# Kernel tuning notes

Hardware: AMD Instinct MI355X
Metric: run time of the kernel (lower is better)

Reference implementation:

```python
import jax, jax.numpy as jnp
import numpy as np

B, C, H, W = 16, 3, 384, 1280
EPS = 1e-7


def setup_inputs() -> dict:
    key = jax.random.key(0)
    k1, k2, k3, k4 = jax.random.split(key, 4)
    source_image = jax.random.normal(k1, (B, C, H, W), jnp.float32)
    depth_map = jax.random.uniform(k2, (B, 1, H, W), jnp.float32, minval=0.1, maxval=80.0)
    pose = 0.05 * jax.random.normal(k3, (B, 6), jnp.float32)
    # realistic KITTI-style pinhole intrinsics, per-batch mild perturbation
    base = jnp.array([[0.58 * W, 0.0, 0.5 * W],
                      [0.0, 1.92 * H, 0.5 * H],
                      [0.0, 0.0, 1.0]], jnp.float32)
    noise = 1.0 + 0.01 * jax.random.normal(k4, (B, 3, 3), jnp.float32)
    intrinsic = base[None] * noise  # zero entries stay zero -> invertible
    return {"source_image": source_image, "depth_map": depth_map,
            "pose": pose, "intrinsic": intrinsic}


def rot_from_axisangle(aa):
    # aa: [B,3] -> [B,3,3] (Rodrigues)
    theta = jnp.linalg.norm(aa, axis=-1, keepdims=True)  # [B,1]
    axis = aa / (theta + EPS)
    c = jnp.cos(theta)
    s = jnp.sin(theta)
    t = 1.0 - c
    x, y, z = axis[:, 0:1], axis[:, 1:2], axis[:, 2:3]
    row0 = jnp.concatenate([t * x * x + c, t * x * y - s * z, t * z * x + s * y], axis=1)
    row1 = jnp.concatenate([t * x * y + s * z, t * y * y + c, t * y * z - s * x], axis=1)
    row2 = jnp.concatenate([t * z * x - s * y, t * y * z + s * x, t * z * z + c], axis=1)
    return jnp.stack([row0, row1, row2], axis=1)  # [B,3,3]


def bilinear_grid_sample(img, gx, gy):
    # img: [B,C,H,W]; gx,gy: [B,H,W] in [-1,1]; align_corners=True, padding zeros
    Bc, Cc, Hc, Wc = img.shape
    x = (gx + 1.0) * 0.5 * (Wc - 1)
    y = (gy + 1.0) * 0.5 * (Hc - 1)
    x0 = jnp.floor(x)
    y0 = jnp.floor(y)
    x1 = x0 + 1.0
    y1 = y0 + 1.0
    wx1 = x - x0
    wx0 = 1.0 - wx1
    wy1 = y - y0
    wy0 = 1.0 - wy1
    imgf = img.reshape(Bc, Cc, Hc * Wc)

    def gather(xi, yi):
        inb = ((xi >= 0) & (xi <= Wc - 1) & (yi >= 0) & (yi <= Hc - 1)).astype(img.dtype)
        xc = jnp.clip(xi, 0, Wc - 1).astype(jnp.int32)
        yc = jnp.clip(yi, 0, Hc - 1).astype(jnp.int32)
        idx = (yc * Wc + xc).reshape(Bc, 1, -1)
        vals = jnp.take_along_axis(imgf, jnp.broadcast_to(idx, (Bc, Cc, idx.shape[-1])), axis=2)
        return vals.reshape(Bc, Cc, Hc, Wc) * inb[:, None]

    out = (gather(x0, y0) * (wx0 * wy0)[:, None]
           + gather(x1, y0) * (wx1 * wy0)[:, None]
           + gather(x0, y1) * (wx0 * wy1)[:, None]
           + gather(x1, y1) * (wx1 * wy1)[:, None])
    return out


def reference(source_image, depth_map, pose, intrinsic):
    Bb, _, Hh, Ww = depth_map.shape
    # pixel grid, homogeneous [H,W,3] = (x, y, 1)
    ys, xs = jnp.meshgrid(jnp.arange(Hh, dtype=depth_map.dtype),
                          jnp.arange(Ww, dtype=depth_map.dtype), indexing='ij')
    pix = jnp.stack([xs, ys, jnp.ones_like(xs)], axis=-1)  # [H,W,3]
    # backproject: K^{-1} @ pix * depth
    inv_K = jnp.linalg.inv(intrinsic)  # [B,3,3]
    cam = jnp.einsum('bij,hwj->bhwi', inv_K, pix)  # [B,H,W,3]
    frustum = cam * jnp.transpose(depth_map, (0, 2, 3, 1))  # [B,H,W,3]
    # rigid transform
    R = rot_from_axisangle(pose[:, :3])  # [B,3,3]
    t = pose[:, 3:]  # [B,3]
    points = jnp.einsum('bij,bhwj->bhwi', R, frustum) + t[:, None, None, :]
    # project with K
    coord = jnp.einsum('bij,bhwj->bhwi', intrinsic, points)  # [B,H,W,3]
    z = coord[..., 2] + EPS
    px = coord[..., 0] / z
    py = coord[..., 1] / z
    gx = px / (Ww - 1) * 2.0 - 1.0
    gy = py / (Hh - 1) * 2.0 - 1.0
    return bilinear_grid_sample(source_image, gx, gy)
```

## Files before the change

### kernel.cpp

```cpp
#include <hip/hip_runtime.h>

#define B_ 16
#define C_ 3
#define H_ 384
#define W_ 1280
#define HW_ (H_*W_)
#define EPS_ 1e-7f

#define COLS_ 256
#define ROWS_ 2
#define BANDS_ (W_/COLS_)
#define RTILES_ (H_/ROWS_)
#define NBLK_ (BANDS_*RTILES_*B_)
#define NXCD_ 8

typedef float v2f __attribute__((ext_vector_type(2)));

__device__ __forceinline__ v2f load2(const float* p) {
  v2f r;
  __builtin_memcpy(&r, p, 8);
  return r;
}

__device__ __forceinline__ void mat3mul(const float* A, const float* Bm, float* C) {
  #pragma unroll
  for (int i = 0; i < 3; i++)
    #pragma unroll
    for (int j = 0; j < 3; j++)
      C[i*3+j] = A[i*3+0]*Bm[0*3+j] + A[i*3+1]*Bm[1*3+j] + A[i*3+2]*Bm[2*3+j];
}

__device__ void compute_MT(const float* __restrict__ pose,
                           const float* __restrict__ intr,
                           int b, float* M, float* T)
{
  float K[9];
  #pragma unroll
  for (int i = 0; i < 9; i++) K[i] = intr[b*9 + i];
  float aa0 = pose[b*6 + 0], aa1 = pose[b*6 + 1], aa2 = pose[b*6 + 2];
  float t0  = pose[b*6 + 3], t1  = pose[b*6 + 4], t2  = pose[b*6 + 5];

  float theta = sqrtf(aa0*aa0 + aa1*aa1 + aa2*aa2);
  float invn  = 1.0f / (theta + EPS_);
  float x = aa0*invn, y = aa1*invn, z = aa2*invn;
  float c = cosf(theta), s = sinf(theta), t = 1.0f - c;
  float R[9] = {
    t*x*x + c,   t*x*y - s*z, t*z*x + s*y,
    t*x*y + s*z, t*y*y + c,   t*y*z - s*x,
    t*z*x - s*y, t*y*z + s*x, t*z*z + c
  };

  float a = K[0], bb = K[1], cc = K[2];
  float d = K[3], e  = K[4], f  = K[5];
  float g = K[6], h  = K[7], ii = K[8];
  float A0 = e*ii - f*h, A1 = f*g - d*ii, A2 = d*h - e*g;
  float id = 1.0f / (a*A0 + bb*A1 + cc*A2);
  float iK[9] = {
    A0*id, (cc*h - bb*ii)*id, (bb*f - cc*e)*id,
    A1*id, (a*ii - cc*g)*id,  (cc*d - a*f)*id,
    A2*id, (bb*g - a*h)*id,   (a*e  - bb*d)*id
  };

  float KR[9];
  mat3mul(K, R, KR);
  mat3mul(KR, iK, M);
  T[0] = K[0]*t0 + K[1]*t1 + K[2]*t2;
  T[1] = K[3]*t0 + K[4]*t1 + K[5]*t2;
  T[2] = K[6]*t0 + K[7]*t1 + K[8]*t2;
}

__global__ __launch_bounds__(256) void warp_kernel(
    const float* __restrict__ src,
    const float* __restrict__ depth,
    const float* __restrict__ pose,
    const float* __restrict__ intr,
    float* __restrict__ out)
{
  __shared__ float sp[12];

  int l = blockIdx.x;
  int w = (l & (NXCD_-1)) * (NBLK_/NXCD_) + (l >> 3);
  int rt   = w % RTILES_;
  int tmp  = w / RTILES_;
  int band = tmp % BANDS_;
  int b    = tmp / BANDS_;

  if (threadIdx.x == 0) {
    float M[9], T[3];
    compute_MT(pose, intr, b, M, T);
    #pragma unroll
    for (int i = 0; i < 9; i++) sp[i] = M[i];
    #pragma unroll
    for (int i = 0; i < 3; i++) sp[9 + i] = T[i];
  }
  __syncthreads();
  float m00 = sp[0], m01 = sp[1], m02 = sp[2];
  float m10 = sp[3], m11 = sp[4], m12 = sp[5];
  float m20 = sp[6], m21 = sp[7], m22 = sp[8];
  float T0  = sp[9], T1  = sp[10], T2 = sp[11];

  int j  = band * COLS_ + threadIdx.x;
  int i0 = rt * ROWS_;
  float xf = (float)j;

  float ax = m00*xf + m02;
  float ay = m10*xf + m12;
  float az = m20*xf + m22;

  size_t sb = (size_t)b * C_ * HW_;
  const float* s0p = src + sb;
  const float* s1p = s0p + HW_;
  const float* s2p = s1p + HW_;

  const float* dp = depth + (size_t)b * HW_ + (size_t)i0 * W_ + j;
  float dv[ROWS_];
  #pragma unroll
  for (int r = 0; r < ROWS_; r++)
    dv[r] = __builtin_nontemporal_load(dp + r * W_);

  #pragma unroll
  for (int r = 0; r < ROWS_; r++) {
    int i = i0 + r;
    float yf = (float)i;
    float d  = dv[r];

    float cx = (ax + m01*yf)*d + T0;
    float cy = (ay + m11*yf)*d + T1;
    float cz = (az + m21*yf)*d + T2;
    float inv = 1.0f / (cz + EPS_);
    float px = cx * inv;
    float py = cy * inv;

    float x0f = floorf(px), y0f = floorf(py);
    float x1f = x0f + 1.0f, y1f = y0f + 1.0f;
    float wx1 = px - x0f, wx0 = 1.0f - wx1;
    float wy1 = py - y0f, wy0 = 1.0f - wy1;

    float mx0 = (x0f >= 0.0f && x0f <= (float)(W_-1)) ? 1.0f : 0.0f;
    float mx1 = (x1f >= 0.0f && x1f <= (float)(W_-1)) ? 1.0f : 0.0f;
    float my0 = (y0f >= 0.0f && y0f <= (float)(H_-1)) ? 1.0f : 0.0f;
    float my1 = (y1f >= 0.0f && y1f <= (float)(H_-1)) ? 1.0f : 0.0f;

    int xc0 = (int)fminf(fmaxf(x0f, 0.0f), (float)(W_-1));
    int xc1 = (int)fminf(fmaxf(x1f, 0.0f), (float)(W_-1));
    int yc0 = (int)fminf(fmaxf(y0f, 0.0f), (float)(H_-1));
    int yc1 = (int)fminf(fmaxf(y1f, 0.0f), (float)(H_-1));

    float w00 = wx0*wy0*mx0*my0;
    float w01 = wx1*wy0*mx1*my0;
    float w10 = wx0*wy1*mx0*my1;
    float w11 = wx1*wy1*mx1*my1;

    int base = xc0 < (W_-2) ? xc0 : (W_-2);
    bool sl0 = (xc0 == base);
    bool sl1 = (xc1 == base + 1);
    float wax = (sl0 ? w00 : 0.0f) + (sl1 ? 0.0f : w01);
    float way = (sl0 ? 0.0f : w00) + (sl1 ? w01 : 0.0f);
    float wbx = (sl0 ? w10 : 0.0f) + (sl1 ? 0.0f : w11);
    float wby = (sl0 ? 0.0f : w10) + (sl1 ? w11 : 0.0f);

    int rb0 = yc0*W_ + base;
    int rb1 = yc1*W_ + base;

    v2f a0 = load2(s0p + rb0);
    v2f b0 = load2(s0p + rb1);
    v2f a1 = load2(s1p + rb0);
    v2f b1 = load2(s1p + rb1);
    v2f a2 = load2(s2p + rb0);
    v2f b2 = load2(s2p + rb1);

    float v0 = a0.x*wax + a0.y*way + b0.x*wbx + b0.y*wby;
    float v1 = a1.x*wax + a1.y*way + b1.x*wbx + b1.y*wby;
    float v2 = a2.x*wax + a2.y*way + b2.x*wbx + b2.y*wby;

    size_t op = (size_t)i * W_ + j;
    __builtin_nontemporal_store(v0, &out[sb + op]);
    __builtin_nontemporal_store(v1, &out[sb + HW_ + op]);
    __builtin_nontemporal_store(v2, &out[sb + 2*(size_t)HW_ + op]);
  }
}

extern "C" void kernel_launch(void* const* d_in, const int* in_sizes, int n_in,
                              void* d_out, int out_size, void* d_ws, size_t ws_size,
                              hipStream_t stream) {
  const float* src   = (const float*)d_in[0];
  const float* depth = (const float*)d_in[1];
  const float* pose  = (const float*)d_in[2];
  const float* intr  = (const float*)d_in[3];
  float* out = (float*)d_out;

  dim3 grid(NBLK_);
  warp_kernel<<<grid, 256, 0, stream>>>(src, depth, pose, intr, out);
}
```

Measured before the change: 251.8 us.

## Process two adjacent pixels per thread sharing a 4-wide source gather window

Each thread now handles two horizontally adjacent output pixels in one row instead of one pixel in each of two rows. A single pair of 4-float source loads per channel serves both bilinear samples, with an extra row load when the second pixel's rows differ and a scalar fallback when its footprint falls outside the window. Depth loads and output stores become 2-wide vectors. The aim is fewer gather instructions and better memory coalescing, at the cost of more select logic, divergent fallback branches and wider 16-byte loads that may be unaligned.

Result: slower. 280.7 us (+11.5%).

```diff
diff --git a/kernel.cpp b/kernel.cpp
--- a/kernel.cpp
+++ b/kernel.cpp
@@ -15,11 +15,20 @@
 #define NXCD_ 8
 
 typedef float v2f __attribute__((ext_vector_type(2)));
+typedef float v4f __attribute__((ext_vector_type(4)));
 
 __device__ __forceinline__ v2f load2(const float* p) {
-  v2f r;
-  __builtin_memcpy(&r, p, 8);
-  return r;
+  v2f r; __builtin_memcpy(&r, p, 8); return r;
+}
+__device__ __forceinline__ v4f load4(const float* p) {
+  v4f r; __builtin_memcpy(&r, p, 16); return r;
+}
+__device__ __forceinline__ void storent2(float* p, float a, float b) {
+  v2f r; r.x = a; r.y = b;
+  __builtin_nontemporal_store(r, (v2f*)p);
+}
+__device__ __forceinline__ float dot4(v4f a, v4f b) {
+  return a.x*b.x + a.y*b.y + a.z*b.z + a.w*b.w;
 }
 
 __device__ __forceinline__ void mat3mul(const float* A, const float* Bm, float* C) {
@@ -69,6 +78,32 @@
   T[2] = K[6]*t0 + K[7]*t1 + K[8]*t2;
 }
 
+__device__ __forceinline__ void project_px(
+    float xf, float yf, float d,
+    float m00,float m01,float m02,float m10,float m11,float m12,
+    float m20,float m21,float m22,float T0,float T1,float T2,
+    float& wx0,float& wx1,float& wy0,float& wy1,
+    int& xc0,int& xc1,int& yc0,int& yc1)
+{
+  float cz = (m20*xf + m21*yf + m22)*d + T2;
+  float inv = 1.0f / (cz + EPS_);
+  float px = ((m00*xf + m01*yf + m02)*d + T0) * inv;
+  float py = ((m10*xf + m11*yf + m12)*d + T1) * inv;
+  float x0f = floorf(px), y0f = floorf(py);
+  float fx1 = px - x0f, fx0 = 1.0f - fx1;
+  float fy1 = py - y0f, fy0 = 1.0f - fy1;
+  float mx0 = (x0f >= 0.0f && x0f <= (float)(W_-1)) ? 1.0f : 0.0f;
+  float mx1 = (x0f+1.0f >= 0.0f && x0f+1.0f <= (float)(W_-1)) ? 1.0f : 0.0f;
+  float my0 = (y0f >= 0.0f && y0f <= (float)(H_-1)) ? 1.0f : 0.0f;
+  float my1 = (y0f+1.0f >= 0.0f && y0f+1.0f <= (float)(H_-1)) ? 1.0f : 0.0f;
+  wx0 = fx0*mx0; wx1 = fx1*mx1;
+  wy0 = fy0*my0; wy1 = fy1*my1;
+  xc0 = (int)fminf(fmaxf(x0f, 0.0f), (float)(W_-1));
+  xc1 = (int)fminf(fmaxf(x0f+1.0f, 0.0f), (float)(W_-1));
+  yc0 = (int)fminf(fmaxf(y0f, 0.0f), (float)(H_-1));
+  yc1 = (int)fminf(fmaxf(y0f+1.0f, 0.0f), (float)(H_-1));
+}
+
 __global__ __launch_bounds__(256) void warp_kernel(
     const float* __restrict__ src,
     const float* __restrict__ depth,
@@ -85,13 +120,22 @@
   int band = tmp % BANDS_;
   int b    = tmp / BANDS_;
 
-  if (threadIdx.x == 0) {
+  int t  = threadIdx.x;
+  int cp = t & 127;
+  int rr = t >> 7;
+  int j0 = band * COLS_ + 2*cp;
+  int i  = rt * ROWS_ + rr;
+
+  const float* dpp = depth + (size_t)b * HW_ + (size_t)i * W_ + j0;
+  v2f dpair = load2(dpp);
+
+  if (t == 0) {
     float M[9], T[3];
     compute_MT(pose, intr, b, M, T);
     #pragma unroll
-    for (int i = 0; i < 9; i++) sp[i] = M[i];
+    for (int k = 0; k < 9; k++) sp[k] = M[k];
     #pragma unroll
-    for (int i = 0; i < 3; i++) sp[9 + i] = T[i];
+    for (int k = 0; k < 3; k++) sp[9 + k] = T[k];
   }
   __syncthreads();
   float m00 = sp[0], m01 = sp[1], m02 = sp[2];
@@ -99,85 +143,86 @@
   float m20 = sp[6], m21 = sp[7], m22 = sp[8];
   float T0  = sp[9], T1  = sp[10], T2 = sp[11];
 
-  int j  = band * COLS_ + threadIdx.x;
-  int i0 = rt * ROWS_;
-  float xf = (float)j;
-
-  float ax = m00*xf + m02;
-  float ay = m10*xf + m12;
-  float az = m20*xf + m22;
+  float yf = (float)i;
+
+  float wxA0,wxA1,wyA0,wyA1, wxB0,wxB1,wyB0,wyB1;
+  int xcA0,xcA1,ycA0,ycA1, xcB0,xcB1,ycB0,ycB1;
+  project_px((float)j0,     yf, dpair.x, m00,m01,m02,m10,m11,m12,m20,m21,m22,T0,T1,T2,
+             wxA0,wxA1,wyA0,wyA1, xcA0,xcA1,ycA0,ycA1);
+  project_px((float)(j0+1), yf, dpair.y, m00,m01,m02,m10,m11,m12,m20,m21,m22,T0,T1,T2,
+             wxB0,wxB1,wyB0,wyB1, xcB0,xcB1,ycB0,ycB1);
+
+  int baseA = xcA0 < (W_-2) ? xcA0 : (W_-2);
+  int bp    = baseA < (W_-4) ? baseA : (W_-4);
+  int pA0 = xcA0 - bp, pA1 = xcA1 - bp;
+  int pB0 = xcB0 - bp, pB1 = xcB1 - bp;
+
+  int R0 = ycA0, R1 = ycA1;
+  int sB0 = (ycB0 == R0) ? 0 : ((ycB0 == R1) ? 1 : 2);
+  int sB1 = (ycB1 == R1) ? 1 : ((ycB1 == R0) ? 0 : 2);
+  bool needE = (sB0 == 2) || (sB1 == 2);
+  bool fb = (pB1 > 3) || (pB0 < 0) || ((sB0 == 2) && (sB1 == 2));
+  int yE = (sB0 == 2) ? ycB0 : ycB1;
+
+  float u0 = (sB0 == 0 ? wyB0 : 0.0f) + (sB1 == 0 ? wyB1 : 0.0f);
+  float u1 = (sB0 == 1 ? wyB0 : 0.0f) + (sB1 == 1 ? wyB1 : 0.0f);
+  float u2 = (sB0 == 2 ? wyB0 : 0.0f) + (sB1 == 2 ? wyB1 : 0.0f);
+
+  v4f wA0v, wA1v, wB0v, wB1v, wB2v;
+  #pragma unroll
+  for (int k = 0; k < 4; k++) {
+    float wva = (pA0 == k ? wxA0 : 0.0f) + (pA1 == k ? wxA1 : 0.0f);
+    float wvb = (pB0 == k ? wxB0 : 0.0f) + (pB1 == k ? wxB1 : 0.0f);
+    wA0v[k] = wva * wyA0;
+    wA1v[k] = wva * wyA1;
+    wB0v[k] = wvb * u0;
+    wB1v[k] = wvb * u1;
+    wB2v[k] = wvb * u2;
+  }
 
   size_t sb = (size_t)b * C_ * HW_;
   const float* s0p = src + sb;
   const float* s1p = s0p + HW_;
   const float* s2p = s1p + HW_;
-
-  const float* dp = depth + (size_t)b * HW_ + (size_t)i0 * W_ + j;
-  float dv[ROWS_];
-  #pragma unroll
-  for (int r = 0; r < ROWS_; r++)
-    dv[r] = __builtin_nontemporal_load(dp + r * W_);
-
-  #pragma unroll
-  for (int r = 0; r < ROWS_; r++) {
-    int i = i0 + r;
-    float yf = (float)i;
-    float d  = dv[r];
-
-    float cx = (ax + m01*yf)*d + T0;
-    float cy = (ay + m11*yf)*d + T1;
-    float cz = (az + m21*yf)*d + T2;
-    float inv = 1.0f / (cz + EPS_);
-    float px = cx * inv;
-    float py = cy * inv;
-
-    float x0f = floorf(px), y0f = floorf(py);
-    float x1f = x0f + 1.0f, y1f = y0f + 1.0f;
-    float wx1 = px - x0f, wx0 = 1.0f - wx1;
-    float wy1 = py - y0f, wy0 = 1.0f - wy1;
-
-    float mx0 = (x0f >= 0.0f && x0f <= (float)(W_-1)) ? 1.0f : 0.0f;
-    float mx1 = (x1f >= 0.0f && x1f <= (float)(W_-1)) ? 1.0f : 0.0f;
-    float my0 = (y0f >= 0.0f && y0f <= (float)(H_-1)) ? 1.0f : 0.0f;
-    float my1 = (y1f >= 0.0f && y1f <= (float)(H_-1)) ? 1.0f : 0.0f;
-
-    int xc0 = (int)fminf(fmaxf(x0f, 0.0f), (float)(W_-1));
-    int xc1 = (int)fminf(fmaxf(x1f, 0.0f), (float)(W_-1));
-    int yc0 = (int)fminf(fmaxf(y0f, 0.0f), (float)(H_-1));
-    int yc1 = (int)fminf(fmaxf(y1f, 0.0f), (float)(H_-1));
-
-    float w00 = wx0*wy0*mx0*my0;
-    float w01 = wx1*wy0*mx1*my0;
-    float w10 = wx0*wy1*mx0*my1;
-    float w11 = wx1*wy1*mx1*my1;
-
-    int base = xc0 < (W_-2) ? xc0 : (W_-2);
-    bool sl0 = (xc0 == base);
-    bool sl1 = (xc1 == base + 1);
-    float wax = (sl0 ? w00 : 0.0f) + (sl1 ? 0.0f : w01);
-    float way = (sl0 ? 0.0f : w00) + (sl1 ? w01 : 0.0f);
-    float wbx = (sl0 ? w10 : 0.0f) + (sl1 ? 0.0f : w11);
-    float wby = (sl0 ? 0.0f : w10) + (sl1 ? w11 : 0.0f);
-
-    int rb0 = yc0*W_ + base;
-    int rb1 = yc1*W_ + base;
-
-    v2f a0 = load2(s0p + rb0);
-    v2f b0 = load2(s0p + rb1);
-    v2f a1 = load2(s1p + rb0);
-    v2f b1 = load2(s1p + rb1);
-    v2f a2 = load2(s2p + rb0);
-    v2f b2 = load2(s2p + rb1);
-
-    float v0 = a0.x*wax + a0.y*way + b0.x*wbx + b0.y*wby;
-    float v1 = a1.x*wax + a1.y*way + b1.x*wbx + b1.y*wby;
-    float v2 = a2.x*wax + a2.y*way + b2.x*wbx + b2.y*wby;
-
-    size_t op = (size_t)i * W_ + j;
-    __builtin_nontemporal_store(v0, &out[sb + op]);
-    __builtin_nontemporal_store(v1, &out[sb + HW_ + op]);
-    __builtin_nontemporal_store(v2, &out[sb + 2*(size_t)HW_ + op]);
-  }
+  int ro0 = R0*W_ + bp;
+  int ro1 = R1*W_ + bp;
+
+  v4f G00 = load4(s0p + ro0);
+  v4f G01 = load4(s0p + ro1);
+  v4f G10 = load4(s1p + ro0);
+  v4f G11 = load4(s1p + ro1);
+  v4f G20 = load4(s2p + ro0);
+  v4f G21 = load4(s2p + ro1);
+
+  v4f E0 = {0.f,0.f,0.f,0.f}, E1 = E0, E2 = E0;
+  if (needE) {
+    int roE = yE*W_ + bp;
+    E0 = load4(s0p + roE);
+    E1 = load4(s1p + roE);
+    E2 = load4(s2p + roE);
+  }
+  __builtin_amdgcn_sched_barrier(0);
+
+  float vA0 = dot4(wA0v, G00) + dot4(wA1v, G01);
+  float vA1 = dot4(wA0v, G10) + dot4(wA1v, G11);
+  float vA2 = dot4(wA0v, G20) + dot4(wA1v, G21);
+  float vB0 = dot4(wB0v, G00) + dot4(wB1v, G01) + dot4(wB2v, E0);
+  float vB1 = dot4(wB0v, G10) + dot4(wB1v, G11) + dot4(wB2v, E1);
+  float vB2 = dot4(wB0v, G20) + dot4(wB1v, G21) + dot4(wB2v, E2);
+
+  if (fb) {
+    float a00 = wxB0*wyB0, a01 = wxB1*wyB0, a10 = wxB0*wyB1, a11 = wxB1*wyB1;
+    int o00 = ycB0*W_ + xcB0, o01 = ycB0*W_ + xcB1;
+    int o10 = ycB1*W_ + xcB0, o11 = ycB1*W_ + xcB1;
+    vB0 = s0p[o00]*a00 + s0p[o01]*a01 + s0p[o10]*a10 + s0p[o11]*a11;
+    vB1 = s1p[o00]*a00 + s1p[o01]*a01 + s1p[o10]*a10 + s1p[o11]*a11;
+    vB2 = s2p[o00]*a00 + s2p[o01]*a01 + s2p[o10]*a10 + s2p[o11]*a11;
+  }
+
+  size_t op = (size_t)i * W_ + j0;
+  storent2(out + sb + op,                    vA0, vB0);
+  storent2(out + sb + HW_ + op,              vA1, vB1);
+  storent2(out + sb + 2*(size_t)HW_ + op,    vA2, vB2);
 }
 
 extern "C" void kernel_launch(void* const* d_in, const int* in_sizes, int n_in,
```

## Process four pixels per thread with vectorized depth loads and output stores

Applied to the files above, without the earlier changes.

Each thread now handles four adjacent pixels in one row instead of one pixel across two rows, with ROWS_ raised to 4 so a block covers 4 rows by 256 columns. Depth is read with a single 16-byte load issued before the barrier, and the three output channels are written as 16-byte vector stores. All 24 gathers are issued together ahead of a scheduling barrier to raise memory-level parallelism. In exchange, register pressure rises, fewer threads work on each row, and the nontemporal hints on the depth load and output stores are gone.

Result: slower. 264.8 us (+5.2%).

```diff
diff --git a/kernel.cpp b/kernel.cpp
--- a/kernel.cpp
+++ b/kernel.cpp
@@ -8,18 +8,21 @@
 #define EPS_ 1e-7f
 
 #define COLS_ 256
-#define ROWS_ 2
+#define ROWS_ 4
+#define PX_ 4
 #define BANDS_ (W_/COLS_)
 #define RTILES_ (H_/ROWS_)
 #define NBLK_ (BANDS_*RTILES_*B_)
 #define NXCD_ 8
 
 typedef float v2f __attribute__((ext_vector_type(2)));
+typedef float v4f __attribute__((ext_vector_type(4)));
 
 __device__ __forceinline__ v2f load2(const float* p) {
-  v2f r;
-  __builtin_memcpy(&r, p, 8);
-  return r;
+  v2f r; __builtin_memcpy(&r, p, 8); return r;
+}
+__device__ __forceinline__ v4f load4(const float* p) {
+  v4f r; __builtin_memcpy(&r, p, 16); return r;
 }
 
 __device__ __forceinline__ void mat3mul(const float* A, const float* Bm, float* C) {
@@ -85,13 +88,21 @@
   int band = tmp % BANDS_;
   int b    = tmp / BANDS_;
 
-  if (threadIdx.x == 0) {
+  int t  = threadIdx.x;
+  int rr = t >> 6;
+  int j0 = band * COLS_ + (t & 63) * PX_;
+  int i  = rt * ROWS_ + rr;
+
+  const float* dpp = depth + (size_t)b * HW_ + (size_t)i * W_ + j0;
+  v4f dq = load4(dpp);
+
+  if (t == 0) {
     float M[9], T[3];
     compute_MT(pose, intr, b, M, T);
     #pragma unroll
-    for (int i = 0; i < 9; i++) sp[i] = M[i];
+    for (int k = 0; k < 9; k++) sp[k] = M[k];
     #pragma unroll
-    for (int i = 0; i < 3; i++) sp[9 + i] = T[i];
+    for (int k = 0; k < 3; k++) sp[9 + k] = T[k];
   }
   __syncthreads();
   float m00 = sp[0], m01 = sp[1], m02 = sp[2];
@@ -99,85 +110,75 @@
   float m20 = sp[6], m21 = sp[7], m22 = sp[8];
   float T0  = sp[9], T1  = sp[10], T2 = sp[11];
 
-  int j  = band * COLS_ + threadIdx.x;
-  int i0 = rt * ROWS_;
-  float xf = (float)j;
-
-  float ax = m00*xf + m02;
-  float ay = m10*xf + m12;
-  float az = m20*xf + m22;
+  float yf = (float)i;
+  float bx = m01*yf + m02;
+  float by = m11*yf + m12;
+  float bz = m21*yf + m22;
 
   size_t sb = (size_t)b * C_ * HW_;
   const float* s0p = src + sb;
   const float* s1p = s0p + HW_;
   const float* s2p = s1p + HW_;
 
-  const float* dp = depth + (size_t)b * HW_ + (size_t)i0 * W_ + j;
-  float dv[ROWS_];
+  float wax[PX_], way[PX_], wbx[PX_], wby[PX_];
+  int rb0[PX_], rb1[PX_];
   #pragma unroll
-  for (int r = 0; r < ROWS_; r++)
-    dv[r] = __builtin_nontemporal_load(dp + r * W_);
-
-  #pragma unroll
-  for (int r = 0; r < ROWS_; r++) {
-    int i = i0 + r;
-    float yf = (float)i;
-    float d  = dv[r];
-
-    float cx = (ax + m01*yf)*d + T0;
-    float cy = (ay + m11*yf)*d + T1;
-    float cz = (az + m21*yf)*d + T2;
+  for (int q = 0; q < PX_; q++) {
+    float xf = (float)(j0 + q);
+    float d  = dq[q];
+    float cz = (m20*xf + bz)*d + T2;
     float inv = 1.0f / (cz + EPS_);
-    float px = cx * inv;
-    float py = cy * inv;
+    float px = ((m00*xf + bx)*d + T0) * inv;
+    float py = ((m10*xf + by)*d + T1) * inv;
 
     float x0f = floorf(px), y0f = floorf(py);
-    float x1f = x0f + 1.0f, y1f = y0f + 1.0f;
-    float wx1 = px - x0f, wx0 = 1.0f - wx1;
-    float wy1 = py - y0f, wy0 = 1.0f - wy1;
+    float fx1 = px - x0f, fx0 = 1.0f - fx1;
+    float fy1 = py - y0f, fy0 = 1.0f - fy1;
+    float wx0 = fx0 * ((x0f >= 0.0f && x0f <= (float)(W_-1)) ? 1.0f : 0.0f);
+    float wx1 = fx1 * ((x0f+1.0f >= 0.0f && x0f+1.0f <= (float)(W_-1)) ? 1.0f : 0.0f);
+    float wy0 = fy0 * ((y0f >= 0.0f && y0f <= (float)(H_-1)) ? 1.0f : 0.0f);
+    float wy1 = fy1 * ((y0f+1.0f >= 0.0f && y0f+1.0f <= (float)(H_-1)) ? 1.0f : 0.0f);
+    int xc0 = (int)fminf(fmaxf(x0f, 0.0f), (float)(W_-1));
+    int xc1 = (int)fminf(fmaxf(x0f+1.0f, 0.0f), (float)(W_-1));
+    int yc0 = (int)fminf(fmaxf(y0f, 0.0f), (float)(H_-1));
+    int yc1 = (int)fminf(fmaxf(y0f+1.0f, 0.0f), (float)(H_-1));
 
-    float mx0 = (x0f >= 0.0f && x0f <= (float)(W_-1)) ? 1.0f : 0.0f;
-    float mx1 = (x1f >= 0.0f && x1f <= (float)(W_-1)) ? 1.0f : 0.0f;
-    float my0 = (y0f >= 0.0f && y0f <= (float)(H_-1)) ? 1.0f : 0.0f;
-    float my1 = (y1f >= 0.0f && y1f <= (float)(H_-1)) ? 1.0f : 0.0f;
+    float w00 = wx0*wy0, w01 = wx1*wy0, w10 = wx0*wy1, w11 = wx1*wy1;
+    int base = xc0 < (W_-2) ? xc0 : (W_-2);
+    bool s0 = (xc0 == base);
+    bool s1 = (xc1 == base + 1);
+    wax[q] = (s0 ? w00 : 0.0f) + (s1 ? 0.0f : w01);
+    way[q] = (s0 ? 0.0f : w00) + (s1 ? w01 : 0.0f);
+    wbx[q] = (s0 ? w10 : 0.0f) + (s1 ? 0.0f : w11);
+    wby[q] = (s0 ? 0.0f : w10) + (s1 ? w11 : 0.0f);
+    rb0[q] = yc0*W_ + base;
+    rb1[q] = yc1*W_ + base;
+  }
 
-    int xc0 = (int)fminf(fmaxf(x0f, 0.0f), (float)(W_-1));
-    int xc1 = (int)fminf(fmaxf(x1f, 0.0f), (float)(W_-1));
-    int yc0 = (int)fminf(fmaxf(y0f, 0.0f), (float)(H_-1));
-    int yc1 = (int)fminf(fmaxf(y1f, 0.0f), (float)(H_-1));
+  v2f gA0[PX_], gB0[PX_], gA1[PX_], gB1[PX_], gA2[PX_], gB2[PX_];
+  #pragma unroll
+  for (int q = 0; q < PX_; q++) {
+    gA0[q] = load2(s0p + rb0[q]);
+    gB0[q] = load2(s0p + rb1[q]);
+    gA1[q] = load2(s1p + rb0[q]);
+    gB1[q] = load2(s1p + rb1[q]);
+    gA2[q] = load2(s2p + rb0[q]);
+    gB2[q] = load2(s2p + rb1[q]);
+  }
+  __builtin_amdgcn_sched_barrier(0);
 
-    float w00 = wx0*wy0*mx0*my0;
-    float w01 = wx1*wy0*mx1*my0;
-    float w10 = wx0*wy1*mx0*my1;
-    float w11 = wx1*wy1*mx1*my1;
+  v4f o0, o1, o2;
+  #pragma unroll
+  for (int q = 0; q < PX_; q++) {
+    o0[q] = gA0[q].x*wax[q] + gA0[q].y*way[q] + gB0[q].x*wbx[q] + gB0[q].y*wby[q];
+    o1[q] = gA1[q].x*wax[q] + gA1[q].y*way[q] + gB1[q].x*wbx[q] + gB1[q].y*wby[q];
+    o2[q] = gA2[q].x*wax[q] + gA2[q].y*way[q] + gB2[q].x*wbx[q] + gB2[q].y*wby[q];
+  }
 
-    int base = xc0 < (W_-2) ? xc0 : (W_-2);
-    bool sl0 = (xc0 == base);
-    bool sl1 = (xc1 == base + 1);
-    float wax = (sl0 ? w00 : 0.0f) + (sl1 ? 0.0f : w01);
-    float way = (sl0 ? 0.0f : w00) + (sl1 ? w01 : 0.0f);
-    float wbx = (sl0 ? w10 : 0.0f) + (sl1 ? 0.0f : w11);
-    float wby = (sl0 ? 0.0f : w10) + (sl1 ? w11 : 0.0f);
-
-    int rb0 = yc0*W_ + base;
-    int rb1 = yc1*W_ + base;
-
-    v2f a0 = load2(s0p + rb0);
-    v2f b0 = load2(s0p + rb1);
-    v2f a1 = load2(s1p + rb0);
-    v2f b1 = load2(s1p + rb1);
-    v2f a2 = load2(s2p + rb0);
-    v2f b2 = load2(s2p + rb1);
-
-    float v0 = a0.x*wax + a0.y*way + b0.x*wbx + b0.y*wby;
-    float v1 = a1.x*wax + a1.y*way + b1.x*wbx + b1.y*wby;
-    float v2 = a2.x*wax + a2.y*way + b2.x*wbx + b2.y*wby;
-
-    size_t op = (size_t)i * W_ + j;
-    __builtin_nontemporal_store(v0, &out[sb + op]);
-    __builtin_nontemporal_store(v1, &out[sb + HW_ + op]);
-    __builtin_nontemporal_store(v2, &out[sb + 2*(size_t)HW_ + op]);
-  }
+  size_t op = (size_t)i * W_ + j0;
+  *(v4f*)(out + sb + op)                  = o0;
+  *(v4f*)(out + sb + HW_ + op)            = o1;
+  *(v4f*)(out + sb + 2*(size_t)HW_ + op)  = o2;
 }
 
 extern "C" void kernel_launch(void* const* d_in, const int* in_sizes, int n_in,
```
